# Optimization experiments

Measured on AMD Instinct MI355X. Metric: run time of the kernel, lower is better.

Reference implementation:

```python
import jax, jax.numpy as jnp
import numpy as np

N = 100000
E = 3200000
IN_DIM = 256
HID = 64
NC = 32
K1 = 2  # conv1 propagation steps
EPS = 1e-5


def setup_inputs() -> dict:
    key = jax.random.key(0)
    ks = jax.random.split(key, 8)
    x = jax.random.normal(ks[0], (N, IN_DIM), dtype=jnp.float32)
    src = jax.random.randint(ks[1], (E,), 0, N)
    dst = jax.random.randint(ks[2], (E,), 0, N)
    W1 = jax.random.normal(ks[3], (IN_DIM, HID), dtype=jnp.float32) / np.sqrt(IN_DIM)
    b1 = jnp.zeros((HID,), dtype=jnp.float32)
    gamma = jnp.ones((HID,), dtype=jnp.float32)
    beta = jnp.zeros((HID,), dtype=jnp.float32)
    W2 = jax.random.normal(ks[4], (HID, NC), dtype=jnp.float32) / np.sqrt(HID)
    b2 = jnp.zeros((NC,), dtype=jnp.float32)
    return {"x": x, "src": src, "dst": dst, "W1": W1, "b1": b1,
            "gamma": gamma, "beta": beta, "W2": W2, "b2": b2}


def _gcn_norm(src, dst, n):
    # deg includes self loop (add_self_loops=True): deg[i] = 1 + in-degree
    deg = jax.ops.segment_sum(jnp.ones_like(src, dtype=jnp.float32), dst, num_segments=n) + 1.0
    dinv = jax.lax.rsqrt(deg)
    w_edge = dinv[src] * dinv[dst]      # [E] normalized edge weights
    w_self = dinv * dinv                # [N] self-loop weights (1/deg)
    return w_edge, w_self


def _propagate(h, src, dst, w_edge, w_self, n):
    # out = D^-1/2 (A+I) D^-1/2 h  via gather-scale-scatter
    msg = w_edge[:, None] * h[src]
    agg = jax.ops.segment_sum(msg, dst, num_segments=n)
    return agg + w_self[:, None] * h


def reference(x, src, dst, W1, b1, gamma, beta, W2, b2):
    n = x.shape[0]
    w_edge, w_self = _gcn_norm(src, dst, n)
    # conv1: K-step propagation then linear
    h = x
    for _ in range(K1):
        h = _propagate(h, src, dst, w_edge, w_self, n)
    h = h @ W1 + b1
    # batchnorm (training-mode batch stats over nodes, biased variance)
    mean = jnp.mean(h, axis=0)
    var = jnp.mean(jnp.square(h - mean), axis=0)
    h = (h - mean) * jax.lax.rsqrt(var + EPS) * gamma + beta
    h = jax.nn.selu(h)
    # dropout p=0.0 -> identity
    # conv2: 1-step propagation then linear
    h = _propagate(h, src, dst, w_edge, w_self, n)
    h = h @ W2 + b2
    return jax.nn.log_softmax(h, axis=1)
```

## Files before the change

### kernel.cpp

```cpp
#include <hip/hip_runtime.h>
#include <hip/hip_fp16.h>

#define NN 100000
#define EE 3200000
#define NB 256
#define NPB 391
#define BCAP 13568
#define NBLK_A 256
#define CHUNK_A (EE / NBLK_A)

#define OFF_AF   0UL
#define OFF_AH   25600000UL
#define OFF_BH   38400000UL
#define OFF_CSR  51200000UL
#define OFF_RP   64000000UL
#define OFF_DINV 64400384UL
#define OFF_SEG  64800768UL
#define OFF_BASE 64808960UL
#define OFF_BN   64813056UL
#define OFF_SS   64813568UL

typedef __attribute__((ext_vector_type(8))) short bf16x8;
typedef __attribute__((ext_vector_type(4))) short short4v;
typedef __attribute__((ext_vector_type(4))) float f32x4;

__global__ __launch_bounds__(256) void passA(const int* __restrict__ src, const int* __restrict__ dst,
                                             int* __restrict__ segcnt, unsigned* __restrict__ buf) {
    __shared__ int hist[NB];
    __shared__ int curl[NB];
    int t = threadIdx.x;
    hist[t] = 0;
    __syncthreads();
    int beg = blockIdx.x * CHUNK_A, end = beg + CHUNK_A;
    for (int i = beg + t; i < end; i += 256)
        atomicAdd(&hist[dst[i] / NPB], 1);
    __syncthreads();
    int h = hist[t];
    int r = atomicAdd(&segcnt[t], h);
    curl[t] = t * BCAP + r;
    __syncthreads();
    for (int i = beg + t; i < end; i += 256) {
        int d = dst[i];
        int k = d / NPB;
        int dl = d - k * NPB;
        int p = atomicAdd(&curl[k], 1);
        if (p < (k + 1) * BCAP)
            buf[p] = ((unsigned)dl << 17) | (unsigned)src[i];
    }
}

__global__ __launch_bounds__(256) void scan_buckets(const int* __restrict__ segcnt,
                                                    int* __restrict__ base, int* __restrict__ rp) {
    __shared__ int s[256];
    int t = threadIdx.x;
    int tot = min(segcnt[t], BCAP);
    s[t] = tot;
    __syncthreads();
    for (int off = 1; off < 256; off <<= 1) {
        int v = (t >= off) ? s[t - off] : 0;
        __syncthreads();
        s[t] += v;
        __syncthreads();
    }
    base[t] = s[t] - tot;
    if (t == 255) { base[256] = s[255]; rp[NN] = s[255]; }
}

__global__ __launch_bounds__(256) void passB(const unsigned* __restrict__ buf,
                                             const int* __restrict__ segcnt,
                                             const int* __restrict__ base,
                                             int* __restrict__ rp, float* __restrict__ dinv,
                                             int* __restrict__ csr) {
    __shared__ unsigned ebuf[BCAP];
    __shared__ int deg_l[NPB];
    __shared__ int off_l[NPB];
    __shared__ int s[256];
    __shared__ int tot0;
    int b = blockIdx.x, t = threadIdx.x;
    int nb = min(segcnt[b], BCAP);
    for (int i = t; i < NPB; i += 256) deg_l[i] = 0;
    const unsigned* sp = buf + (size_t)b * BCAP;
    for (int j = t; j < nb; j += 256) ebuf[j] = sp[j];
    __syncthreads();
    for (int j = t; j < nb; j += 256) atomicAdd(&deg_l[ebuf[j] >> 17], 1);
    __syncthreads();
    int d0 = deg_l[t];
    s[t] = d0;
    __syncthreads();
    for (int off = 1; off < 256; off <<= 1) {
        int v = (t >= off) ? s[t - off] : 0;
        __syncthreads();
        s[t] += v;
        __syncthreads();
    }
    off_l[t] = s[t] - d0;
    if (t == 255) tot0 = s[255];
    __syncthreads();
    int i1 = 256 + t;
    int d1 = (i1 < NPB) ? deg_l[i1] : 0;
    s[t] = d1;
    __syncthreads();
    for (int off = 1; off < 256; off <<= 1) {
        int v = (t >= off) ? s[t - off] : 0;
        __syncthreads();
        s[t] += v;
        __syncthreads();
    }
    if (i1 < NPB) off_l[i1] = tot0 + s[t] - d1;
    __syncthreads();
    int nodebase = b * NPB;
    int cbase = base[b];
    for (int i = t; i < NPB; i += 256) {
        int node = nodebase + i;
        if (node < NN) {
            rp[node] = cbase + off_l[i];
            dinv[node] = rsqrtf((float)deg_l[i] + 1.0f);
        }
    }
    __syncthreads();
    for (int j = t; j < nb; j += 256) {
        unsigned e = ebuf[j];
        int p = atomicAdd(&off_l[e >> 17], 1);
        csr[cbase + p] = (int)(e & 0x1FFFFu);
    }
}

__global__ __launch_bounds__(256) void wprep(const float* __restrict__ W1, short* __restrict__ wf) {
    int e = blockIdx.x * 256 + threadIdx.x;
    if (e >= 16384) return;
    int j = e & 7, lane = (e >> 3) & 63, nt = (e >> 9) & 3, ks = e >> 11;
    int k = ks * 32 + (lane >> 4) * 8 + j;
    int col = nt * 16 + (lane & 15);
    float w = W1[k * 64 + col];
    unsigned b = __float_as_uint(w);
    short hi = (short)(b >> 16);
    float hf = __uint_as_float(b & 0xFFFF0000u);
    float lo = w - hf;
    short lov = (short)(__float_as_uint(lo) >> 16);
    wf[((size_t)(ks * 8 + nt * 2 + 0) * 64 + lane) * 8 + j] = hi;
    wf[((size_t)(ks * 8 + nt * 2 + 1) * 64 + lane) * 8 + j] = lov;
}

__global__ __launch_bounds__(256) void gemm1(const float* __restrict__ x, const short* __restrict__ wf,
                                             const float* __restrict__ dinv, __half* __restrict__ Ah) {
    __shared__ short xh[64 * 256];
    __shared__ short xl[64 * 256];
    int t = threadIdx.x;
    int row0b = blockIdx.x * 64;
    int nrows = NN - row0b < 64 ? NN - row0b : 64;
    const float4* xg = (const float4*)(x + (size_t)row0b * 256);
    int n4 = nrows * 64;
    for (int i = t; i < n4; i += 256) {
        float4 v = xg[i];
        int row = i >> 6, kq = i & 63;
        unsigned bx = __float_as_uint(v.x), by = __float_as_uint(v.y);
        unsigned bz = __float_as_uint(v.z), bw = __float_as_uint(v.w);
        short4v hv, lv;
        hv.x = (short)(bx >> 16); hv.y = (short)(by >> 16);
        hv.z = (short)(bz >> 16); hv.w = (short)(bw >> 16);
        float lx = v.x - __uint_as_float(bx & 0xFFFF0000u);
        float ly = v.y - __uint_as_float(by & 0xFFFF0000u);
        float lz = v.z - __uint_as_float(bz & 0xFFFF0000u);
        float lw = v.w - __uint_as_float(bw & 0xFFFF0000u);
        lv.x = (short)(__float_as_uint(lx) >> 16); lv.y = (short)(__float_as_uint(ly) >> 16);
        lv.z = (short)(__float_as_uint(lz) >> 16); lv.w = (short)(__float_as_uint(lw) >> 16);
        unsigned off = ((unsigned)(row * 512 + kq * 8)) ^ ((unsigned)(row & 7) << 4);
        *(short4v*)((char*)xh + off) = hv;
        *(short4v*)((char*)xl + off) = lv;
    }
    __syncthreads();
    int wid = t >> 6, lane = t & 63;
    int r0 = wid * 16;
    f32x4 acc[4];
    #pragma unroll
    for (int nt = 0; nt < 4; ++nt) acc[nt] = (f32x4){0.f, 0.f, 0.f, 0.f};
    int lrow = r0 + (lane & 15);
    int kgrp = (lane >> 4) * 8;
    for (int ks = 0; ks < 8; ++ks) {
        unsigned xoff = ((unsigned)(lrow * 512 + (ks * 32 + kgrp) * 2)) ^ ((unsigned)(lrow & 7) << 4);
        bf16x8 a_hi = *(const bf16x8*)((const char*)xh + xoff);
        bf16x8 a_lo = *(const bf16x8*)((const char*)xl + xoff);
        const short* wfk = wf + (size_t)(ks * 8) * 64 * 8;
        #pragma unroll
        for (int nt = 0; nt < 4; ++nt) {
            bf16x8 b_hi = *(const bf16x8*)(wfk + ((nt * 2 + 0) * 64 + lane) * 8);
            bf16x8 b_lo = *(const bf16x8*)(wfk + ((nt * 2 + 1) * 64 + lane) * 8);
            acc[nt] = __builtin_amdgcn_mfma_f32_16x16x32_bf16(a_hi, b_hi, acc[nt], 0, 0, 0);
            acc[nt] = __builtin_amdgcn_mfma_f32_16x16x32_bf16(a_hi, b_lo, acc[nt], 0, 0, 0);
            acc[nt] = __builtin_amdgcn_mfma_f32_16x16x32_bf16(a_lo, b_hi, acc[nt], 0, 0, 0);
        }
    }
    int mb = (lane >> 4) * 4;
    #pragma unroll
    for (int reg = 0; reg < 4; ++reg) {
        int row = row0b + r0 + mb + reg;
        if (row < NN) {
            float dv = dinv[row];
            #pragma unroll
            for (int nt = 0; nt < 4; ++nt)
                Ah[(size_t)row * 64 + nt * 16 + (lane & 15)] = __float2half(acc[nt][reg] * dv);
        }
    }
}

template <int P>
__global__ __launch_bounds__(256) void agg64h(const __half* __restrict__ h, void* __restrict__ outv,
                                              const int* __restrict__ rp, const int* __restrict__ csr,
                                              const float* __restrict__ dinv) {
    int lane = threadIdx.x & 63;
    int node = (blockIdx.x << 2) + (threadIdx.x >> 6);
    if (node >= NN) return;
    int hid = lane >> 5;
    int c2 = (lane & 31) * 2;
    float dd = dinv[node];
    float ax = 0.f, ay = 0.f, bx = 0.f, by = 0.f;
    if (hid == 0) {
        __half2 sv = *(const __half2*)(h + (size_t)node * 64 + c2);
        ax = __half2float(sv.x); ay = __half2float(sv.y);
    }
    int beg = rp[node], end = rp[node + 1];
    for (int j0 = beg; j0 < end; j0 += 64) {
        int m = end - j0; if (m > 64) m = 64;
        int s = csr[j0 + (lane < m ? lane : 0)];
        int j = 0;
        for (; j + 7 < m; j += 8) {
            int i0 = __shfl(s, j + hid);
            int i1 = __shfl(s, j + 2 + hid);
            int i2 = __shfl(s, j + 4 + hid);
            int i3 = __shfl(s, j + 6 + hid);
            __half2 v0 = *(const __half2*)(h + (size_t)i0 * 64 + c2);
            __half2 v1 = *(const __half2*)(h + (size_t)i1 * 64 + c2);
            __half2 v2 = *(const __half2*)(h + (size_t)i2 * 64 + c2);
            __half2 v3 = *(const __half2*)(h + (size_t)i3 * 64 + c2);
            ax += __half2float(v0.x); ay += __half2float(v0.y);
            bx += __half2float(v1.x); by += __half2float(v1.y);
            ax += __half2float(v2.x); ay += __half2float(v2.y);
            bx += __half2float(v3.x); by += __half2float(v3.y);
        }
        for (; j < m; j += 2) {
            int idx = j + hid;
            int cidx = idx < m ? idx : m - 1;
            int sj = __shfl(s, cidx);
            if (idx < m) {
                __half2 v = *(const __half2*)(h + (size_t)sj * 64 + c2);
                ax += __half2float(v.x); ay += __half2float(v.y);
            }
        }
    }
    float sx = ax + bx, sy = ay + by;
    sx += __shfl(sx, lane ^ 32);
    sy += __shfl(sy, lane ^ 32);
    if (hid == 0) {
        if (P == 2) {
            float w = dd * dd;
            __half2 o;
            o.x = __float2half(sx * w); o.y = __float2half(sy * w);
            *(__half2*)((__half*)outv + (size_t)node * 64 + c2) = o;
        } else {
            *(float2*)((float*)outv + (size_t)node * 64 + c2) = make_float2(sx * dd, sy * dd);
        }
    }
}

__global__ __launch_bounds__(256) void agg32f(const __half* __restrict__ U, float* __restrict__ outp,
                                              const int* __restrict__ rp, const int* __restrict__ csr,
                                              const float* __restrict__ dinv, const float* __restrict__ b2) {
    int lane = threadIdx.x & 63;
    int node = (blockIdx.x << 2) + (threadIdx.x >> 6);
    if (node >= NN) return;
    int gid = lane >> 4;
    int c2 = (lane & 15) * 2;
    float dd = dinv[node];
    float ax = 0.f, ay = 0.f;
    if (gid == 0) {
        __half2 sv = *(const __half2*)(U + (size_t)node * 32 + c2);
        ax = __half2float(sv.x); ay = __half2float(sv.y);
    }
    int beg = rp[node], end = rp[node + 1];
    for (int j0 = beg; j0 < end; j0 += 64) {
        int m = end - j0; if (m > 64) m = 64;
        int s = csr[j0 + (lane < m ? lane : 0)];
        int j = 0;
        for (; j + 7 < m; j += 8) {
            int i0 = __shfl(s, j + gid);
            int i1 = __shfl(s, j + 4 + gid);
            __half2 v0 = *(const __half2*)(U + (size_t)i0 * 32 + c2);
            __half2 v1 = *(const __half2*)(U + (size_t)i1 * 32 + c2);
            ax += __half2float(v0.x) + __half2float(v1.x);
            ay += __half2float(v0.y) + __half2float(v1.y);
        }
        for (; j < m; j += 4) {
            int idx = j + gid;
            int cidx = idx < m ? idx : m - 1;
            int sj = __shfl(s, cidx);
            if (idx < m) {
                __half2 v = *(const __half2*)(U + (size_t)sj * 32 + c2);
                ax += __half2float(v.x); ay += __half2float(v.y);
            }
        }
    }
    ax += __shfl(ax, lane ^ 16); ay += __shfl(ay, lane ^ 16);
    ax += __shfl(ax, lane ^ 32); ay += __shfl(ay, lane ^ 32);
    float v0 = ax * dd + b2[c2];
    float v1 = ay * dd + b2[c2 + 1];
    float mx = fmaxf(v0, v1);
    mx = fmaxf(mx, __shfl_xor(mx, 1));
    mx = fmaxf(mx, __shfl_xor(mx, 2));
    mx = fmaxf(mx, __shfl_xor(mx, 4));
    mx = fmaxf(mx, __shfl_xor(mx, 8));
    float sum = __expf(v0 - mx) + __expf(v1 - mx);
    sum += __shfl_xor(sum, 1);
    sum += __shfl_xor(sum, 2);
    sum += __shfl_xor(sum, 4);
    sum += __shfl_xor(sum, 8);
    if (gid == 0) {
        float ls = __logf(sum);
        *(float2*)(outp + (size_t)node * 32 + c2) = make_float2(v0 - mx - ls, v1 - mx - ls);
    }
}

__global__ __launch_bounds__(256) void bn_stats(const float* __restrict__ A, float* __restrict__ bn) {
    int t = threadIdx.x;
    int c = t & 63, rg = t >> 6;
    float s = 0.f, sq = 0.f;
    for (int r = blockIdx.x * 4 + rg; r < NN; r += gridDim.x * 4) {
        float v = A[(size_t)r * 64 + c];
        s += v; sq += v * v;
    }
    __shared__ float ls[256], lq[256];
    ls[t] = s; lq[t] = sq;
    __syncthreads();
    if (t < 64) {
        float S = ls[t] + ls[t + 64] + ls[t + 128] + ls[t + 192];
        float Q = lq[t] + lq[t + 64] + lq[t + 128] + lq[t + 192];
        atomicAdd(&bn[t], S);
        atomicAdd(&bn[64 + t], Q);
    }
}

__global__ void bn_final(const float* __restrict__ bn, const float* __restrict__ gamma,
                         const float* __restrict__ beta, float* __restrict__ ss) {
    int c = threadIdx.x;
    float mean = bn[c] / (float)NN;
    float var = bn[64 + c] / (float)NN - mean * mean;
    float sc = gamma[c] * rsqrtf(var + 1e-5f);
    ss[c] = sc;
    ss[64 + c] = beta[c] - mean * sc;
}

__global__ __launch_bounds__(256) void gemm2(const float* __restrict__ A, const float* __restrict__ W2,
                                             const float* __restrict__ ss, const float* __restrict__ dinv,
                                             __half* __restrict__ U) {
    __shared__ float w2s[64 * 32];
    __shared__ float sc[64], sh[64];
    for (int i = threadIdx.x; i < 512; i += 256)
        ((float4*)w2s)[i] = ((const float4*)W2)[i];
    if (threadIdx.x < 64) {
        sc[threadIdx.x] = ss[threadIdx.x];
        sh[threadIdx.x] = ss[64 + threadIdx.x];
    }
    __syncthreads();
    const float SELU_S = 1.0507009873554805f;
    const float SELU_AS = 1.7580993408473766f;
    int lane = threadIdx.x & 31, grp = threadIdx.x >> 5;
    int node = blockIdx.x * 8 + grp;
    if (node >= NN) return;
    const float* Ar = A + (size_t)node * 64;
    float v0 = Ar[lane];
    float v1 = Ar[lane + 32];
    v0 = v0 * sc[lane] + sh[lane];
    v1 = v1 * sc[lane + 32] + sh[lane + 32];
    v0 = v0 > 0.f ? SELU_S * v0 : SELU_AS * (__expf(v0) - 1.0f);
    v1 = v1 > 0.f ? SELU_S * v1 : SELU_AS * (__expf(v1) - 1.0f);
    float acc = 0.f;
    #pragma unroll
    for (int j = 0; j < 32; ++j) {
        acc += __shfl(v0, j, 32) * w2s[j * 32 + lane];
        acc += __shfl(v1, j, 32) * w2s[(j + 32) * 32 + lane];
    }
    U[(size_t)node * 32 + lane] = __float2half(dinv[node] * acc);
}

extern "C" void kernel_launch(void* const* d_in, const int* in_sizes, int n_in,
                              void* d_out, int out_size, void* d_ws, size_t ws_size,
                              hipStream_t stream) {
    const float* x     = (const float*)d_in[0];
    const int*   src   = (const int*)d_in[1];
    const int*   dst   = (const int*)d_in[2];
    const float* W1    = (const float*)d_in[3];
    const float* gamma = (const float*)d_in[5];
    const float* beta  = (const float*)d_in[6];
    const float* W2    = (const float*)d_in[7];
    const float* b2    = (const float*)d_in[8];
    float* out = (float*)d_out;

    char* ws = (char*)d_ws;
    float*    Af   = (float*)(ws + OFF_AF);
    unsigned* bbuf = (unsigned*)(ws + OFF_AF);
    __half*   Ah   = (__half*)(ws + OFF_AH);
    __half*   Bh   = (__half*)(ws + OFF_BH);
    short*    wf   = (short*)(ws + OFF_BH);
    __half*   Uh   = (__half*)(ws + OFF_BH);
    int*      csr  = (int*)(ws + OFF_CSR);
    int*      rp   = (int*)(ws + OFF_RP);
    float*    dinv = (float*)(ws + OFF_DINV);
    int*      seg  = (int*)(ws + OFF_SEG);
    int*      base = (int*)(ws + OFF_BASE);
    float*    bn   = (float*)(ws + OFF_BN);
    float*    ssb  = (float*)(ws + OFF_SS);

    hipMemsetAsync(seg, 0, NB * sizeof(int), stream);
    hipMemsetAsync(bn, 0, 128 * sizeof(float), stream);

    wprep<<<64, 256, 0, stream>>>(W1, wf);

    passA<<<NBLK_A, 256, 0, stream>>>(src, dst, seg, bbuf);
    scan_buckets<<<1, 256, 0, stream>>>(seg, base, rp);
    passB<<<NB, 256, 0, stream>>>(bbuf, seg, base, rp, dinv, csr);

    gemm1<<<(NN + 63) / 64, 256, 0, stream>>>(x, wf, dinv, Ah);
    agg64h<2><<<NN / 4, 256, 0, stream>>>(Ah, (void*)Bh, rp, csr, dinv);
    agg64h<1><<<NN / 4, 256, 0, stream>>>(Bh, (void*)Af, rp, csr, dinv);

    bn_stats<<<1024, 256, 0, stream>>>(Af, bn);
    bn_final<<<1, 64, 0, stream>>>(bn, gamma, beta, ssb);

    gemm2<<<NN / 8, 256, 0, stream>>>(Af, W2, ssb, dinv, Uh);
    agg32f<<<NN / 4, 256, 0, stream>>>(Uh, out, rp, csr, dinv, b2);
}
```

Measured before the change: 395.3 us.

## Load x directly into registers in gemm1, store A in fp16, unroll gathers

gemm1 drops its shared-memory staging. Each wave now loads its 16 rows of x straight into registers and splits them into bf16 hi/lo pairs, so there is no LDS traffic or block-wide sync, but the global loads are now strided per lane. The second aggregation writes the post-conv1 activations as fp16 instead of fp32, which halves the traffic read back by bn_stats and gemm2 and adds rounding error before batchnorm. The gather loops in agg64h and agg32f get a 16-wide unrolled stage to keep more independent loads in flight.

```diff
diff --git a/kernel.cpp b/kernel.cpp
--- a/kernel.cpp
+++ b/kernel.cpp
@@ -21,7 +21,6 @@
 #define OFF_SS   64813568UL
 
 typedef __attribute__((ext_vector_type(8))) short bf16x8;
-typedef __attribute__((ext_vector_type(4))) short short4v;
 typedef __attribute__((ext_vector_type(4))) float f32x4;
 
 __global__ __launch_bounds__(256) void passA(const int* __restrict__ src, const int* __restrict__ dst,
@@ -143,43 +142,28 @@
 
 __global__ __launch_bounds__(256) void gemm1(const float* __restrict__ x, const short* __restrict__ wf,
                                              const float* __restrict__ dinv, __half* __restrict__ Ah) {
-    __shared__ short xh[64 * 256];
-    __shared__ short xl[64 * 256];
-    int t = threadIdx.x;
-    int row0b = blockIdx.x * 64;
-    int nrows = NN - row0b < 64 ? NN - row0b : 64;
-    const float4* xg = (const float4*)(x + (size_t)row0b * 256);
-    int n4 = nrows * 64;
-    for (int i = t; i < n4; i += 256) {
-        float4 v = xg[i];
-        int row = i >> 6, kq = i & 63;
-        unsigned bx = __float_as_uint(v.x), by = __float_as_uint(v.y);
-        unsigned bz = __float_as_uint(v.z), bw = __float_as_uint(v.w);
-        short4v hv, lv;
-        hv.x = (short)(bx >> 16); hv.y = (short)(by >> 16);
-        hv.z = (short)(bz >> 16); hv.w = (short)(bw >> 16);
-        float lx = v.x - __uint_as_float(bx & 0xFFFF0000u);
-        float ly = v.y - __uint_as_float(by & 0xFFFF0000u);
-        float lz = v.z - __uint_as_float(bz & 0xFFFF0000u);
-        float lw = v.w - __uint_as_float(bw & 0xFFFF0000u);
-        lv.x = (short)(__float_as_uint(lx) >> 16); lv.y = (short)(__float_as_uint(ly) >> 16);
-        lv.z = (short)(__float_as_uint(lz) >> 16); lv.w = (short)(__float_as_uint(lw) >> 16);
-        unsigned off = ((unsigned)(row * 512 + kq * 8)) ^ ((unsigned)(row & 7) << 4);
-        *(short4v*)((char*)xh + off) = hv;
-        *(short4v*)((char*)xl + off) = lv;
-    }
-    __syncthreads();
-    int wid = t >> 6, lane = t & 63;
-    int r0 = wid * 16;
+    int wid = threadIdx.x >> 6, lane = threadIdx.x & 63;
+    int g = blockIdx.x * 4 + wid;
+    if (g >= NN / 16) return;
+    int lrow = g * 16 + (lane & 15);
+    int kgrp = (lane >> 4) * 8;
+    const float* xp = x + (size_t)lrow * 256 + kgrp;
     f32x4 acc[4];
     #pragma unroll
     for (int nt = 0; nt < 4; ++nt) acc[nt] = (f32x4){0.f, 0.f, 0.f, 0.f};
-    int lrow = r0 + (lane & 15);
-    int kgrp = (lane >> 4) * 8;
     for (int ks = 0; ks < 8; ++ks) {
-        unsigned xoff = ((unsigned)(lrow * 512 + (ks * 32 + kgrp) * 2)) ^ ((unsigned)(lrow & 7) << 4);
-        bf16x8 a_hi = *(const bf16x8*)((const char*)xh + xoff);
-        bf16x8 a_lo = *(const bf16x8*)((const char*)xl + xoff);
+        float4 f0 = *(const float4*)(xp + ks * 32);
+        float4 f1 = *(const float4*)(xp + ks * 32 + 4);
+        bf16x8 a_hi, a_lo;
+        const float* fp = &f0.x;
+        #pragma unroll
+        for (int j = 0; j < 8; ++j) {
+            float f = (j < 4) ? fp[j] : (&f1.x)[j - 4];
+            unsigned b = __float_as_uint(f);
+            a_hi[j] = (short)(b >> 16);
+            float lo = f - __uint_as_float(b & 0xFFFF0000u);
+            a_lo[j] = (short)(__float_as_uint(lo) >> 16);
+        }
         const short* wfk = wf + (size_t)(ks * 8) * 64 * 8;
         #pragma unroll
         for (int nt = 0; nt < 4; ++nt) {
@@ -193,18 +177,16 @@
     int mb = (lane >> 4) * 4;
     #pragma unroll
     for (int reg = 0; reg < 4; ++reg) {
-        int row = row0b + r0 + mb + reg;
-        if (row < NN) {
-            float dv = dinv[row];
-            #pragma unroll
-            for (int nt = 0; nt < 4; ++nt)
-                Ah[(size_t)row * 64 + nt * 16 + (lane & 15)] = __float2half(acc[nt][reg] * dv);
-        }
+        int row = g * 16 + mb + reg;
+        float dv = dinv[row];
+        #pragma unroll
+        for (int nt = 0; nt < 4; ++nt)
+            Ah[(size_t)row * 64 + nt * 16 + (lane & 15)] = __float2half(acc[nt][reg] * dv);
     }
 }
 
 template <int P>
-__global__ __launch_bounds__(256) void agg64h(const __half* __restrict__ h, void* __restrict__ outv,
+__global__ __launch_bounds__(256) void agg64h(const __half* __restrict__ h, __half* __restrict__ outp,
                                               const int* __restrict__ rp, const int* __restrict__ csr,
                                               const float* __restrict__ dinv) {
     int lane = threadIdx.x & 63;
@@ -223,6 +205,32 @@
         int m = end - j0; if (m > 64) m = 64;
         int s = csr[j0 + (lane < m ? lane : 0)];
         int j = 0;
+        for (; j + 15 < m; j += 16) {
+            int i0 = __shfl(s, j + hid);
+            int i1 = __shfl(s, j + 2 + hid);
+            int i2 = __shfl(s, j + 4 + hid);
+            int i3 = __shfl(s, j + 6 + hid);
+            int i4 = __shfl(s, j + 8 + hid);
+            int i5 = __shfl(s, j + 10 + hid);
+            int i6 = __shfl(s, j + 12 + hid);
+            int i7 = __shfl(s, j + 14 + hid);
+            __half2 v0 = *(const __half2*)(h + (size_t)i0 * 64 + c2);
+            __half2 v1 = *(const __half2*)(h + (size_t)i1 * 64 + c2);
+            __half2 v2 = *(const __half2*)(h + (size_t)i2 * 64 + c2);
+            __half2 v3 = *(const __half2*)(h + (size_t)i3 * 64 + c2);
+            __half2 v4 = *(const __half2*)(h + (size_t)i4 * 64 + c2);
+            __half2 v5 = *(const __half2*)(h + (size_t)i5 * 64 + c2);
+            __half2 v6 = *(const __half2*)(h + (size_t)i6 * 64 + c2);
+            __half2 v7 = *(const __half2*)(h + (size_t)i7 * 64 + c2);
+            ax += __half2float(v0.x) + __half2float(v2.x);
+            ay += __half2float(v0.y) + __half2float(v2.y);
+            bx += __half2float(v1.x) + __half2float(v3.x);
+            by += __half2float(v1.y) + __half2float(v3.y);
+            ax += __half2float(v4.x) + __half2float(v6.x);
+            ay += __half2float(v4.y) + __half2float(v6.y);
+            bx += __half2float(v5.x) + __half2float(v7.x);
+            by += __half2float(v5.y) + __half2float(v7.y);
+        }
         for (; j + 7 < m; j += 8) {
             int i0 = __shfl(s, j + hid);
             int i1 = __shfl(s, j + 2 + hid);
@@ -232,10 +240,10 @@
             __half2 v1 = *(const __half2*)(h + (size_t)i1 * 64 + c2);
             __half2 v2 = *(const __half2*)(h + (size_t)i2 * 64 + c2);
             __half2 v3 = *(const __half2*)(h + (size_t)i3 * 64 + c2);
-            ax += __half2float(v0.x); ay += __half2float(v0.y);
-            bx += __half2float(v1.x); by += __half2float(v1.y);
-            ax += __half2float(v2.x); ay += __half2float(v2.y);
-            bx += __half2float(v3.x); by += __half2float(v3.y);
+            ax += __half2float(v0.x) + __half2float(v2.x);
+            ay += __half2float(v0.y) + __half2float(v2.y);
+            bx += __half2float(v1.x) + __half2float(v3.x);
+            by += __half2float(v1.y) + __half2float(v3.y);
         }
         for (; j < m; j += 2) {
             int idx = j + hid;
@@ -251,14 +259,10 @@
     sx += __shfl(sx, lane ^ 32);
     sy += __shfl(sy, lane ^ 32);
     if (hid == 0) {
-        if (P == 2) {
-            float w = dd * dd;
-            __half2 o;
-            o.x = __float2half(sx * w); o.y = __float2half(sy * w);
-            *(__half2*)((__half*)outv + (size_t)node * 64 + c2) = o;
-        } else {
-            *(float2*)((float*)outv + (size_t)node * 64 + c2) = make_float2(sx * dd, sy * dd);
-        }
+        float w = (P == 2) ? dd * dd : dd;
+        __half2 o;
+        o.x = __float2half(sx * w); o.y = __float2half(sy * w);
+        *(__half2*)(outp + (size_t)node * 64 + c2) = o;
     }
 }
 
@@ -281,6 +285,18 @@
         int m = end - j0; if (m > 64) m = 64;
         int s = csr[j0 + (lane < m ? lane : 0)];
         int j = 0;
+        for (; j + 15 < m; j += 16) {
+            int i0 = __shfl(s, j + gid);
+            int i1 = __shfl(s, j + 4 + gid);
+            int i2 = __shfl(s, j + 8 + gid);
+            int i3 = __shfl(s, j + 12 + gid);
+            __half2 v0 = *(const __half2*)(U + (size_t)i0 * 32 + c2);
+            __half2 v1 = *(const __half2*)(U + (size_t)i1 * 32 + c2);
+            __half2 v2 = *(const __half2*)(U + (size_t)i2 * 32 + c2);
+            __half2 v3 = *(const __half2*)(U + (size_t)i3 * 32 + c2);
+            ax += __half2float(v0.x) + __half2float(v1.x) + __half2float(v2.x) + __half2float(v3.x);
+            ay += __half2float(v0.y) + __half2float(v1.y) + __half2float(v2.y) + __half2float(v3.y);
+        }
         for (; j + 7 < m; j += 8) {
             int i0 = __shfl(s, j + gid);
             int i1 = __shfl(s, j + 4 + gid);
@@ -319,12 +335,12 @@
     }
 }
 
-__global__ __launch_bounds__(256) void bn_stats(const float* __restrict__ A, float* __restrict__ bn) {
+__global__ __launch_bounds__(256) void bn_stats(const __half* __restrict__ A, float* __restrict__ bn) {
     int t = threadIdx.x;
     int c = t & 63, rg = t >> 6;
     float s = 0.f, sq = 0.f;
     for (int r = blockIdx.x * 4 + rg; r < NN; r += gridDim.x * 4) {
-        float v = A[(size_t)r * 64 + c];
+        float v = __half2float(A[(size_t)r * 64 + c]);
         s += v; sq += v * v;
     }
     __shared__ float ls[256], lq[256];
@@ -348,7 +364,7 @@
     ss[64 + c] = beta[c] - mean * sc;
 }
 
-__global__ __launch_bounds__(256) void gemm2(const float* __restrict__ A, const float* __restrict__ W2,
+__global__ __launch_bounds__(256) void gemm2(const __half* __restrict__ A, const float* __restrict__ W2,
                                              const float* __restrict__ ss, const float* __restrict__ dinv,
                                              __half* __restrict__ U) {
     __shared__ float w2s[64 * 32];
@@ -365,9 +381,9 @@
     int lane = threadIdx.x & 31, grp = threadIdx.x >> 5;
     int node = blockIdx.x * 8 + grp;
     if (node >= NN) return;
-    const float* Ar = A + (size_t)node * 64;
-    float v0 = Ar[lane];
-    float v1 = Ar[lane + 32];
+    const __half* Ar = A + (size_t)node * 64;
+    float v0 = __half2float(Ar[lane]);
+    float v1 = __half2float(Ar[lane + 32]);
     v0 = v0 * sc[lane] + sh[lane];
     v1 = v1 * sc[lane + 32] + sh[lane + 32];
     v0 = v0 > 0.f ? SELU_S * v0 : SELU_AS * (__expf(v0) - 1.0f);
@@ -395,7 +411,7 @@
     float* out = (float*)d_out;
 
     char* ws = (char*)d_ws;
-    float*    Af   = (float*)(ws + OFF_AF);
+    __half*   Af   = (__half*)(ws + OFF_AF);
     unsigned* bbuf = (unsigned*)(ws + OFF_AF);
     __half*   Ah   = (__half*)(ws + OFF_AH);
     __half*   Bh   = (__half*)(ws + OFF_BH);
@@ -418,9 +434,9 @@
     scan_buckets<<<1, 256, 0, stream>>>(seg, base, rp);
     passB<<<NB, 256, 0, stream>>>(bbuf, seg, base, rp, dinv, csr);
 
-    gemm1<<<(NN + 63) / 64, 256, 0, stream>>>(x, wf, dinv, Ah);
-    agg64h<2><<<NN / 4, 256, 0, stream>>>(Ah, (void*)Bh, rp, csr, dinv);
-    agg64h<1><<<NN / 4, 256, 0, stream>>>(Bh, (void*)Af, rp, csr, dinv);
+    gemm1<<<(NN / 16 + 3) / 4, 256, 0, stream>>>(x, wf, dinv, Ah);
+    agg64h<2><<<NN / 4, 256, 0, stream>>>(Ah, Bh, rp, csr, dinv);
+    agg64h<1><<<NN / 4, 256, 0, stream>>>(Bh, Af, rp, csr, dinv);
 
     bn_stats<<<1024, 256, 0, stream>>>(Af, bn);
     bn_final<<<1, 64, 0, stream>>>(bn, gamma, beta, ssb);
```

Measured after the change: 358.2 us. -9.4%, faster.
